# Optimization experiments

Measured on AMD Instinct MI355X. Metric: run time of the kernel, lower is better.

## Reference

```python
import jax, jax.numpy as jnp
import numpy as np

B, S, D = 1, 4096, 768
H = 12
HD = D // H  # 64


def setup_inputs() -> dict:
    key = jax.random.key(0)
    ks = jax.random.split(key, 6)
    sd = 1.0 / np.sqrt(D)
    return {
        "inputs": jax.random.normal(ks[0], (B, S, D), dtype=jnp.float32),
        "Wq": jax.random.uniform(ks[1], (D, D), jnp.float32, -sd, sd),
        "Wk": jax.random.uniform(ks[2], (D, D), jnp.float32, -sd, sd),
        "Wv": jax.random.uniform(ks[3], (D, D), jnp.float32, -sd, sd),
        "Wo": jax.random.uniform(ks[4], (D, D), jnp.float32, -sd, sd),
        "bo": jax.random.uniform(ks[5], (D,), jnp.float32, -sd, sd),
    }


def reference(inputs, Wq, Wk, Wv, Wo, bo):
    b, n, _ = inputs.shape
    # Linear layers (torch Linear: x @ W.T); W stored as [d_out, d_in]-equivalent here as [D, D] applied via x @ W.T
    q = inputs @ Wq.T  # [b, n, D]
    k = inputs @ Wk.T
    v = inputs @ Wv.T
    # [b, H, n, HD]
    q = q.reshape(b, n, H, HD).transpose(0, 2, 1, 3)
    k = k.reshape(b, n, H, HD).transpose(0, 2, 1, 3)
    v = v.reshape(b, n, H, HD).transpose(0, 2, 1, 3)
    scores = jnp.einsum("bhqd,bhkd->bhqk", q, k)
    causal = jnp.triu(jnp.ones((n, n), dtype=bool), k=1)
    scores = jnp.where(causal, -jnp.inf, scores)
    attn = jax.nn.softmax(scores / np.sqrt(HD), axis=-1)  # dropout p=0.0 -> identity
    ctx = jnp.einsum("bhqk,bhkd->bhqd", attn, v)
    ctx = ctx.transpose(0, 2, 1, 3).reshape(b, n, D)
    return ctx @ Wo.T + bo
```

## Files before the change

kernel.cpp:

```cpp
#include <hip/hip_runtime.h>
#include <math.h>

static constexpr int S_LEN  = 4096;
static constexpr int DMODEL = 768;
static constexpr int NHEAD  = 12;
static constexpr int HDIM   = 64;

typedef __attribute__((ext_vector_type(8))) short   bf16x8;
typedef __attribute__((ext_vector_type(4))) float   f32x4;
typedef __attribute__((ext_vector_type(8))) unsigned short us8;

__device__ __forceinline__ unsigned short f2b(float f) {
  union { float f; unsigned int u; } v; v.f = f;
  unsigned int u = v.u;
  return (unsigned short)((u + 0x7fffu + ((u >> 16) & 1u)) >> 16);
}

__device__ __forceinline__ float dpp_max16(float x) {
  float y;
  y = __int_as_float(__builtin_amdgcn_mov_dpp(__float_as_int(x), 0xB1, 0xf, 0xf, true)); x = fmaxf(x, y);
  y = __int_as_float(__builtin_amdgcn_mov_dpp(__float_as_int(x), 0x4E, 0xf, 0xf, true)); x = fmaxf(x, y);
  y = __int_as_float(__builtin_amdgcn_mov_dpp(__float_as_int(x), 0x124, 0xf, 0xf, true)); x = fmaxf(x, y);
  y = __int_as_float(__builtin_amdgcn_mov_dpp(__float_as_int(x), 0x128, 0xf, 0xf, true)); x = fmaxf(x, y);
  return x;
}
__device__ __forceinline__ float dpp_sum16(float x) {
  float y;
  y = __int_as_float(__builtin_amdgcn_mov_dpp(__float_as_int(x), 0xB1, 0xf, 0xf, true)); x += y;
  y = __int_as_float(__builtin_amdgcn_mov_dpp(__float_as_int(x), 0x4E, 0xf, 0xf, true)); x += y;
  y = __int_as_float(__builtin_amdgcn_mov_dpp(__float_as_int(x), 0x124, 0xf, 0xf, true)); x += y;
  y = __int_as_float(__builtin_amdgcn_mov_dpp(__float_as_int(x), 0x128, 0xf, 0xf, true)); x += y;
  return x;
}

__global__ __launch_bounds__(256)
void cvt_f2b_kern(const float* __restrict__ in, unsigned short* __restrict__ out, int n) {
  int i = (blockIdx.x * blockDim.x + threadIdx.x) * 8;
  if (i >= n) return;
  float4 a = *(const float4*)(in + i);
  float4 b = *(const float4*)(in + i + 4);
  ushort4 o0; o0.x = f2b(a.x); o0.y = f2b(a.y); o0.z = f2b(a.z); o0.w = f2b(a.w);
  ushort4 o1; o1.x = f2b(b.x); o1.y = f2b(b.y); o1.z = f2b(b.z); o1.w = f2b(b.w);
  *(ushort4*)(out + i)     = o0;
  *(ushort4*)(out + i + 4) = o1;
}

__global__ __launch_bounds__(256)
void cvt_f2b4_kern(const float* __restrict__ s0, const float* __restrict__ s1,
                   const float* __restrict__ s2, const float* __restrict__ s3,
                   unsigned short* __restrict__ d0, unsigned short* __restrict__ d1,
                   unsigned short* __restrict__ d2, unsigned short* __restrict__ d3,
                   int n) {
  const float* s; unsigned short* d;
  switch (blockIdx.y) {
    case 0: s = s0; d = d0; break;
    case 1: s = s1; d = d1; break;
    case 2: s = s2; d = d2; break;
    default: s = s3; d = d3; break;
  }
  int i = (blockIdx.x * blockDim.x + threadIdx.x) * 8;
  if (i >= n) return;
  float4 a = *(const float4*)(s + i);
  float4 b = *(const float4*)(s + i + 4);
  ushort4 o0; o0.x = f2b(a.x); o0.y = f2b(a.y); o0.z = f2b(a.z); o0.w = f2b(a.w);
  ushort4 o1; o1.x = f2b(b.x); o1.y = f2b(b.y); o1.z = f2b(b.z); o1.w = f2b(b.w);
  *(ushort4*)(d + i)     = o0;
  *(ushort4*)(d + i + 4) = o1;
}

__global__ __launch_bounds__(256)
void transpose_bf16(const unsigned short* __restrict__ in, unsigned short* __restrict__ out) {
  __shared__ __align__(16) unsigned short Ts[64][72];
  const int d0 = blockIdx.x * 64, s0 = blockIdx.y * 64;
  const int r = threadIdx.x >> 2, q = threadIdx.x & 3;
#pragma unroll
  for (int hh = 0; hh < 2; ++hh) {
    const int c8 = q + hh * 4;
    us8 v = *(const us8*)(in + (size_t)(s0 + r) * DMODEL + d0 + c8 * 8);
    *(us8*)(&Ts[r][c8 * 8]) = v;
  }
  __syncthreads();
#pragma unroll
  for (int hh = 0; hh < 2; ++hh) {
    const int sq = q + hh * 4;
    __align__(16) unsigned short tmp[8];
#pragma unroll
    for (int j = 0; j < 8; ++j) tmp[j] = Ts[sq * 8 + j][r];
    *(us8*)(out + (size_t)(d0 + r) * S_LEN + s0 + sq * 8) = *(us8*)tmp;
  }
}

template<int OUT_MODE>
__device__ __forceinline__
void gemm_body(const unsigned short* __restrict__ A, const unsigned short* __restrict__ B,
               const float* __restrict__ bias, void* __restrict__ Cout,
               int M, int N, int K, float scale, int bx, int by,
               unsigned short* As, unsigned short* Bs) {
  const int l  = threadIdx.x & 63;
  const int w  = threadIdx.x >> 6;
  const int wm = (w >> 1) * 32, wn = (w & 1) * 32;
  const int m0 = by * 64;
  const int n0 = bx * 64;
  const int lr = l & 15, lg = l >> 4;
  const int sr = threadIdx.x >> 2, sq = threadIdx.x & 3;

  f32x4 acc[2][2] = {};
  us8 areg[2], breg[2];

#pragma unroll
  for (int p = 0; p < 2; ++p) {
    const int c = sq + p * 4;
    areg[p] = *(const us8*)(A + (size_t)(m0 + sr) * K + c * 8);
    breg[p] = *(const us8*)(B + (size_t)(n0 + sr) * K + c * 8);
  }
#pragma unroll
  for (int p = 0; p < 2; ++p) {
    const int c = sq + p * 4;
    const int slot = ((c ^ (sr & 7)) * 8);
    *(us8*)(&As[sr * 64 + slot]) = areg[p];
    *(us8*)(&Bs[sr * 64 + slot]) = breg[p];
  }
  __syncthreads();

  const int nsteps = K / 64;
  for (int t = 0; t < nsteps; ++t) {
    const bool more = (t + 1 < nsteps);
    if (more) {
      const int kn = (t + 1) * 64;
#pragma unroll
      for (int p = 0; p < 2; ++p) {
        const int c = sq + p * 4;
        areg[p] = *(const us8*)(A + (size_t)(m0 + sr) * K + kn + c * 8);
        breg[p] = *(const us8*)(B + (size_t)(n0 + sr) * K + kn + c * 8);
      }
    }
#pragma unroll
    for (int kc = 0; kc < 2; ++kc) {
      const int cr = kc * 4 + lg;
      bf16x8 af[2], bfr[2];
#pragma unroll
      for (int mi = 0; mi < 2; ++mi) {
        const int row = wm + mi * 16 + lr;
        af[mi] = *(const bf16x8*)(&As[row * 64 + ((cr ^ (row & 7)) * 8)]);
      }
#pragma unroll
      for (int ni = 0; ni < 2; ++ni) {
        const int row = wn + ni * 16 + lr;
        bfr[ni] = *(const bf16x8*)(&Bs[row * 64 + ((cr ^ (row & 7)) * 8)]);
      }
#pragma unroll
      for (int mi = 0; mi < 2; ++mi)
#pragma unroll
        for (int ni = 0; ni < 2; ++ni)
          acc[mi][ni] = __builtin_amdgcn_mfma_f32_16x16x32_bf16(af[mi], bfr[ni], acc[mi][ni], 0, 0, 0);
    }
    __syncthreads();
    if (more) {
#pragma unroll
      for (int p = 0; p < 2; ++p) {
        const int c = sq + p * 4;
        const int slot = ((c ^ (sr & 7)) * 8);
        *(us8*)(&As[sr * 64 + slot]) = areg[p];
        *(us8*)(&Bs[sr * 64 + slot]) = breg[p];
      }
      __syncthreads();
    }
  }

  const int orow = (l >> 4) * 4;
#pragma unroll
  for (int mi = 0; mi < 2; ++mi)
#pragma unroll
    for (int ni = 0; ni < 2; ++ni) {
      const int col = n0 + wn + ni * 16 + lr;
      float bb = (OUT_MODE == 1) ? bias[col] : 0.f;
#pragma unroll
      for (int r = 0; r < 4; ++r) {
        const int row = m0 + wm + mi * 16 + orow + r;
        float v = acc[mi][ni][r] * scale;
        if (OUT_MODE == 0)
          ((unsigned short*)Cout)[(size_t)row * N + col] = f2b(v);
        else
          ((float*)Cout)[(size_t)row * N + col] = v + bb;
      }
    }
}

__global__ __launch_bounds__(256)
void gemm_qkv_lds(const unsigned short* __restrict__ X,
                  const unsigned short* __restrict__ Wq, const unsigned short* __restrict__ Wk,
                  const unsigned short* __restrict__ Wv,
                  unsigned short* __restrict__ Qh, unsigned short* __restrict__ Kh,
                  unsigned short* __restrict__ Vh) {
  __shared__ __align__(16) unsigned short As[64 * 64];
  __shared__ __align__(16) unsigned short Bs[64 * 64];
  const unsigned short* B; unsigned short* C; float scale;
  switch (blockIdx.z) {
    case 0:  B = Wq; C = Qh; scale = 0.125f; break;
    case 1:  B = Wk; C = Kh; scale = 1.0f;   break;
    default: B = Wv; C = Vh; scale = 1.0f;   break;
  }
  gemm_body<0>(X, B, nullptr, C, S_LEN, DMODEL, DMODEL, scale,
               blockIdx.x, blockIdx.y, As, Bs);
}

__global__ __launch_bounds__(256)
void gemm_lds_f32(const unsigned short* __restrict__ A, const unsigned short* __restrict__ B,
                  const float* __restrict__ bias, float* __restrict__ C) {
  __shared__ __align__(16) unsigned short As[64 * 64];
  __shared__ __align__(16) unsigned short Bs[64 * 64];
  gemm_body<1>(A, B, bias, C, S_LEN, DMODEL, DMODEL, 1.0f,
               blockIdx.x, blockIdx.y, As, Bs);
}

__global__ __launch_bounds__(256, 3)
void attn_fwd_mfma(const unsigned short* __restrict__ Q, const unsigned short* __restrict__ K,
                   const unsigned short* __restrict__ Vt, unsigned short* __restrict__ O) {
  __shared__ __align__(16) unsigned short Ks[2][64 * 64];
  __shared__ __align__(16) unsigned short Vs[2][64 * 64];
  __shared__ __align__(16) unsigned short Ps[4][2 * 16 * 64];

  const int item = blockIdx.x;
  int s;
  if (item < 256)      s = item;
  else if (item < 512) s = 767 - item;
  else                 s = item;
  const int qt = 63 - s / NHEAD;
  const int h  = s % NHEAD;
  const int q0 = qt * 64;
  const int tid = threadIdx.x;
  const int w = tid >> 6, l = tid & 63;
  const int lr = l & 15, lg = l >> 4;
  const int sr = tid >> 2, sq = tid & 3;

  bf16x8 qf[2];
#pragma unroll
  for (int kc = 0; kc < 2; ++kc)
    qf[kc] = *(const bf16x8*)(Q + (size_t)(q0 + w * 16 + lr) * DMODEL + h * HDIM + kc * 32 + lg * 8);

  f32x4 o_acc[4] = {};
  float m_i[4], l_i[4];
#pragma unroll
  for (int r = 0; r < 4; ++r) { m_i[r] = -1e30f; l_i[r] = 0.f; }

  const int nt2    = (qt + 2) >> 1;
  const int ntFull = (64 * qt >= 127) ? ((64 * qt - 127) / 128 + 1) : 0;

  us8 kreg[2][2], vreg[2][2];

#pragma unroll
  for (int hh = 0; hh < 2; ++hh)
#pragma unroll
    for (int p = 0; p < 2; ++p) {
      const int qw = sq + p * 4;
      kreg[hh][p] = *(const us8*)(K  + (size_t)(hh * 64 + sr) * DMODEL + h * HDIM + qw * 8);
      vreg[hh][p] = *(const us8*)(Vt + (size_t)(h * HDIM + sr) * S_LEN + hh * 64 + qw * 8);
    }
#pragma unroll
  for (int hh = 0; hh < 2; ++hh)
#pragma unroll
    for (int p = 0; p < 2; ++p) {
      const int qw = sq + p * 4;
      const int sw = (qw * 8) ^ ((sr & 7) * 8);
      *(us8*)(&Ks[hh][sr * 64 + sw]) = kreg[hh][p];
      *(us8*)(&Vs[hh][sr * 64 + sw]) = vreg[hh][p];
    }
  __syncthreads();

  for (int t = 0; t < nt2; ++t) {
    const int k0 = t * 128;
    const bool more = (t + 1 < nt2);
    const bool need_mask = (t >= ntFull);

    if (more) {
      const int k0n = k0 + 128;
#pragma unroll
      for (int hh = 0; hh < 2; ++hh)
#pragma unroll
        for (int p = 0; p < 2; ++p) {
          const int qw = sq + p * 4;
          kreg[hh][p] = *(const us8*)(K  + (size_t)(k0n + hh * 64 + sr) * DMODEL + h * HDIM + qw * 8);
          vreg[hh][p] = *(const us8*)(Vt + (size_t)(h * HDIM + sr) * S_LEN + k0n + hh * 64 + qw * 8);
        }
    }

    f32x4 sacc[2][4] = {};
#pragma unroll
    for (int hh = 0; hh < 2; ++hh)
#pragma unroll
      for (int kc = 0; kc < 2; ++kc)
#pragma unroll
        for (int cb = 0; cb < 4; ++cb) {
          const int kv = cb * 16 + lr;
          bf16x8 kf = *(const bf16x8*)(&Ks[hh][kv * 64 + ((kc * 32 + lg * 8) ^ ((kv & 7) * 8))]);
          sacc[hh][cb] = __builtin_amdgcn_mfma_f32_16x16x32_bf16(qf[kc], kf, sacc[hh][cb], 0, 0, 0);
        }

    float p[4][8];
#pragma unroll
    for (int r = 0; r < 4; ++r) {
      const int qg = q0 + w * 16 + lg * 4 + r;
      float sv[8];
#pragma unroll
      for (int hh = 0; hh < 2; ++hh)
#pragma unroll
        for (int cb = 0; cb < 4; ++cb)
          sv[hh * 4 + cb] = sacc[hh][cb][r];
      if (need_mask) {
#pragma unroll
        for (int hh = 0; hh < 2; ++hh)
#pragma unroll
          for (int cb = 0; cb < 4; ++cb) {
            const int kg = k0 + hh * 64 + cb * 16 + lr;
            if (kg > qg) sv[hh * 4 + cb] = -1e30f;
          }
      }
      float mt = fmaxf(fmaxf(fmaxf(sv[0], sv[1]), fmaxf(sv[2], sv[3])),
                       fmaxf(fmaxf(sv[4], sv[5]), fmaxf(sv[6], sv[7])));
      mt = dpp_max16(mt);
      const float mnew = fmaxf(m_i[r], mt);
      const float alpha = __expf(m_i[r] - mnew);
      m_i[r] = mnew;
      float rs = 0.f;
#pragma unroll
      for (int e = 0; e < 8; ++e) { p[r][e] = __expf(sv[e] - mnew); rs += p[r][e]; }
      rs = dpp_sum16(rs);
      l_i[r] = l_i[r] * alpha + rs;
#pragma unroll
      for (int db = 0; db < 4; ++db) o_acc[db][r] *= alpha;
    }

#pragma unroll
    for (int r = 0; r < 4; ++r) {
      const int qloc = lg * 4 + r;
#pragma unroll
      for (int hh = 0; hh < 2; ++hh)
#pragma unroll
        for (int cb = 0; cb < 4; ++cb) {
          const int kvl = cb * 16 + lr;
          Ps[w][hh * 1024 + qloc * 64 + (kvl ^ ((qloc & 7) * 8))] = f2b(p[r][hh * 4 + cb]);
        }
    }

#pragma unroll
    for (int hh = 0; hh < 2; ++hh)
#pragma unroll
      for (int kc = 0; kc < 2; ++kc) {
        bf16x8 pf = *(const bf16x8*)(&Ps[w][hh * 1024 + lr * 64 + ((kc * 32 + lg * 8) ^ ((lr & 7) * 8))]);
#pragma unroll
        for (int db = 0; db < 4; ++db) {
          const int d = db * 16 + lr;
          bf16x8 vf = *(const bf16x8*)(&Vs[hh][d * 64 + ((kc * 32 + lg * 8) ^ ((d & 7) * 8))]);
          o_acc[db] = __builtin_amdgcn_mfma_f32_16x16x32_bf16(pf, vf, o_acc[db], 0, 0, 0);
        }
      }

    __syncthreads();
    if (more) {
#pragma unroll
      for (int hh = 0; hh < 2; ++hh)
#pragma unroll
        for (int p = 0; p < 2; ++p) {
          const int qw = sq + p * 4;
          const int sw = (qw * 8) ^ ((sr & 7) * 8);
          *(us8*)(&Ks[hh][sr * 64 + sw]) = kreg[hh][p];
          *(us8*)(&Vs[hh][sr * 64 + sw]) = vreg[hh][p];
        }
      __syncthreads();
    }
  }

#pragma unroll
  for (int r = 0; r < 4; ++r) {
    const float inv = 1.f / l_i[r];
    const int row = q0 + w * 16 + lg * 4 + r;
#pragma unroll
    for (int db = 0; db < 4; ++db)
      O[(size_t)row * DMODEL + h * HDIM + db * 16 + lr] = f2b(o_acc[db][r] * inv);
  }
}

extern "C" void kernel_launch(void* const* d_in, const int* in_sizes, int n_in,
                              void* d_out, int out_size, void* d_ws, size_t ws_size,
                              hipStream_t stream) {
  const float* x  = (const float*)d_in[0];
  const float* Wq = (const float*)d_in[1];
  const float* Wk = (const float*)d_in[2];
  const float* Wv = (const float*)d_in[3];
  const float* Wo = (const float*)d_in[4];
  const float* bo = (const float*)d_in[5];
  float* out = (float*)d_out;

  const size_t SD = (size_t)S_LEN * DMODEL;
  const size_t DD = (size_t)DMODEL * DMODEL;

  unsigned short* xh   = (unsigned short*)d_ws;
  unsigned short* Wqh  = xh   + SD;
  unsigned short* Wkh  = Wqh  + DD;
  unsigned short* Wvh  = Wkh  + DD;
  unsigned short* Woh  = Wvh  + DD;
  unsigned short* Qh   = Woh  + DD;
  unsigned short* Kh   = Qh   + SD;
  unsigned short* Vh   = Kh   + SD;
  unsigned short* Vth  = Vh   + SD;
  unsigned short* ctxh = Vth  + SD;

  const dim3 blk(256);

  cvt_f2b_kern<<<dim3((int)(SD / 8 / 256)), blk, 0, stream>>>(x, xh, (int)SD);
  cvt_f2b4_kern<<<dim3((int)(DD / 8 / 256), 4), blk, 0, stream>>>(
      Wq, Wk, Wv, Wo, Wqh, Wkh, Wvh, Woh, (int)DD);

  gemm_qkv_lds<<<dim3(DMODEL / 64, S_LEN / 64, 3), blk, 0, stream>>>(
      xh, Wqh, Wkh, Wvh, Qh, Kh, Vh);

  transpose_bf16<<<dim3(DMODEL / 64, S_LEN / 64), blk, 0, stream>>>(Vh, Vth);

  attn_fwd_mfma<<<dim3(S_LEN / 64 * NHEAD), blk, 0, stream>>>(Qh, Kh, Vth, ctxh);

  gemm_lds_f32<<<dim3(DMODEL / 64, S_LEN / 64), blk, 0, stream>>>(ctxh, Woh, bo, out);
}
```

Before: 140.2 us.

## Use 128-row query tiles with 8 waves per attention block

Each attention block now covers 128 query rows with 512 threads (8 waves) instead of 64 rows with 256 threads, so every K/V tile loaded into LDS is reused by twice as many query rows and global K/V traffic is halved. The cooperative loads now use 8 lanes per row, and the block-to-tile mapping is changed to balance causal work across a grid half as large. Every tile now spans the full 128-key step, so only the diagonal tile needs masking, but fewer, larger blocks may reduce occupancy and load balance.

```diff
diff --git a/kernel.cpp b/kernel.cpp
--- a/kernel.cpp
+++ b/kernel.cpp
@@ -213,75 +213,66 @@
                blockIdx.x, blockIdx.y, As, Bs);
 }
 
-__global__ __launch_bounds__(256, 3)
+__global__ __launch_bounds__(512, 2)
 void attn_fwd_mfma(const unsigned short* __restrict__ Q, const unsigned short* __restrict__ K,
                    const unsigned short* __restrict__ Vt, unsigned short* __restrict__ O) {
   __shared__ __align__(16) unsigned short Ks[2][64 * 64];
   __shared__ __align__(16) unsigned short Vs[2][64 * 64];
-  __shared__ __align__(16) unsigned short Ps[4][2 * 16 * 64];
-
-  const int item = blockIdx.x;
-  int s;
-  if (item < 256)      s = item;
-  else if (item < 512) s = 767 - item;
-  else                 s = item;
-  const int qt = 63 - s / NHEAD;
-  const int h  = s % NHEAD;
-  const int q0 = qt * 64;
+  __shared__ __align__(16) unsigned short Ps[8][2 * 16 * 64];
+
+  const int pos = blockIdx.x;
+  int rank;
+  if (pos < 128)       rank = 128 + pos;
+  else if (pos < 256)  rank = pos - 128;
+  else                 rank = 383 - (pos - 256);
+  const int qtile = 31 - rank / NHEAD;
+  const int h     = rank % NHEAD;
+  const int q0b   = qtile * 128;
+
   const int tid = threadIdx.x;
   const int w = tid >> 6, l = tid & 63;
   const int lr = l & 15, lg = l >> 4;
-  const int sr = tid >> 2, sq = tid & 3;
+  const int sr = tid >> 3, sq = tid & 7;
 
   bf16x8 qf[2];
 #pragma unroll
   for (int kc = 0; kc < 2; ++kc)
-    qf[kc] = *(const bf16x8*)(Q + (size_t)(q0 + w * 16 + lr) * DMODEL + h * HDIM + kc * 32 + lg * 8);
+    qf[kc] = *(const bf16x8*)(Q + (size_t)(q0b + w * 16 + lr) * DMODEL + h * HDIM + kc * 32 + lg * 8);
 
   f32x4 o_acc[4] = {};
   float m_i[4], l_i[4];
 #pragma unroll
   for (int r = 0; r < 4; ++r) { m_i[r] = -1e30f; l_i[r] = 0.f; }
 
-  const int nt2    = (qt + 2) >> 1;
-  const int ntFull = (64 * qt >= 127) ? ((64 * qt - 127) / 128 + 1) : 0;
-
-  us8 kreg[2][2], vreg[2][2];
-
-#pragma unroll
-  for (int hh = 0; hh < 2; ++hh)
-#pragma unroll
-    for (int p = 0; p < 2; ++p) {
-      const int qw = sq + p * 4;
-      kreg[hh][p] = *(const us8*)(K  + (size_t)(hh * 64 + sr) * DMODEL + h * HDIM + qw * 8);
-      vreg[hh][p] = *(const us8*)(Vt + (size_t)(h * HDIM + sr) * S_LEN + hh * 64 + qw * 8);
-    }
-#pragma unroll
-  for (int hh = 0; hh < 2; ++hh)
-#pragma unroll
-    for (int p = 0; p < 2; ++p) {
-      const int qw = sq + p * 4;
-      const int sw = (qw * 8) ^ ((sr & 7) * 8);
-      *(us8*)(&Ks[hh][sr * 64 + sw]) = kreg[hh][p];
-      *(us8*)(&Vs[hh][sr * 64 + sw]) = vreg[hh][p];
-    }
+  const int nt = qtile + 1;
+
+  us8 kreg[2], vreg[2];
+
+#pragma unroll
+  for (int hh = 0; hh < 2; ++hh) {
+    kreg[hh] = *(const us8*)(K  + (size_t)(hh * 64 + sr) * DMODEL + h * HDIM + sq * 8);
+    vreg[hh] = *(const us8*)(Vt + (size_t)(h * HDIM + sr) * S_LEN + hh * 64 + sq * 8);
+  }
+#pragma unroll
+  for (int hh = 0; hh < 2; ++hh) {
+    const int sw = (sq * 8) ^ ((sr & 7) * 8);
+    *(us8*)(&Ks[hh][sr * 64 + sw]) = kreg[hh];
+    *(us8*)(&Vs[hh][sr * 64 + sw]) = vreg[hh];
+  }
   __syncthreads();
 
-  for (int t = 0; t < nt2; ++t) {
+  for (int t = 0; t < nt; ++t) {
     const int k0 = t * 128;
-    const bool more = (t + 1 < nt2);
-    const bool need_mask = (t >= ntFull);
+    const bool more = (t + 1 < nt);
+    const bool need_mask = (t == qtile);
 
     if (more) {
       const int k0n = k0 + 128;
 #pragma unroll
-      for (int hh = 0; hh < 2; ++hh)
-#pragma unroll
-        for (int p = 0; p < 2; ++p) {
-          const int qw = sq + p * 4;
-          kreg[hh][p] = *(const us8*)(K  + (size_t)(k0n + hh * 64 + sr) * DMODEL + h * HDIM + qw * 8);
-          vreg[hh][p] = *(const us8*)(Vt + (size_t)(h * HDIM + sr) * S_LEN + k0n + hh * 64 + qw * 8);
-        }
+      for (int hh = 0; hh < 2; ++hh) {
+        kreg[hh] = *(const us8*)(K  + (size_t)(k0n + hh * 64 + sr) * DMODEL + h * HDIM + sq * 8);
+        vreg[hh] = *(const us8*)(Vt + (size_t)(h * HDIM + sr) * S_LEN + k0n + hh * 64 + sq * 8);
+      }
     }
 
     f32x4 sacc[2][4] = {};
@@ -299,7 +290,7 @@
     float p[4][8];
 #pragma unroll
     for (int r = 0; r < 4; ++r) {
-      const int qg = q0 + w * 16 + lg * 4 + r;
+      const int qg = q0b + w * 16 + lg * 4 + r;
       float sv[8];
 #pragma unroll
       for (int hh = 0; hh < 2; ++hh)
@@ -358,14 +349,11 @@
     __syncthreads();
     if (more) {
 #pragma unroll
-      for (int hh = 0; hh < 2; ++hh)
-#pragma unroll
-        for (int p = 0; p < 2; ++p) {
-          const int qw = sq + p * 4;
-          const int sw = (qw * 8) ^ ((sr & 7) * 8);
-          *(us8*)(&Ks[hh][sr * 64 + sw]) = kreg[hh][p];
-          *(us8*)(&Vs[hh][sr * 64 + sw]) = vreg[hh][p];
-        }
+      for (int hh = 0; hh < 2; ++hh) {
+        const int sw = (sq * 8) ^ ((sr & 7) * 8);
+        *(us8*)(&Ks[hh][sr * 64 + sw]) = kreg[hh];
+        *(us8*)(&Vs[hh][sr * 64 + sw]) = vreg[hh];
+      }
       __syncthreads();
     }
   }
@@ -373,7 +361,7 @@
 #pragma unroll
   for (int r = 0; r < 4; ++r) {
     const float inv = 1.f / l_i[r];
-    const int row = q0 + w * 16 + lg * 4 + r;
+    const int row = q0b + w * 16 + lg * 4 + r;
 #pragma unroll
     for (int db = 0; db < 4; ++db)
       O[(size_t)row * DMODEL + h * HDIM + db * 16 + lr] = f2b(o_acc[db][r] * inv);
@@ -416,7 +404,7 @@
 
   transpose_bf16<<<dim3(DMODEL / 64, S_LEN / 64), blk, 0, stream>>>(Vh, Vth);
 
-  attn_fwd_mfma<<<dim3(S_LEN / 64 * NHEAD), blk, 0, stream>>>(Qh, Kh, Vth, ctxh);
+  attn_fwd_mfma<<<dim3(S_LEN / 128 * NHEAD), dim3(512), 0, stream>>>(Qh, Kh, Vth, ctxh);
 
   gemm_lds_f32<<<dim3(DMODEL / 64, S_LEN / 64), blk, 0, stream>>>(ctxh, Woh, bo, out);
 }
```

Result: slower. 151.0 us (+7.7%).

## Fold log2e into Q scale, use exp2, and skip rescale with lazy max

Applied to the files above, without the earlier changes.

The Q projection scale now includes log2(e), so the attention softmax can use the native exp2 instruction instead of __expf. The online-softmax rescale of the running output and sum is skipped wave-wide whenever every row's new tile max stays within 8 of the running max, which avoids per-tile alpha multiplies. Global-to-LDS loads are also remapped so each thread reads two adjacent 16-byte chunks instead of strided ones. The lazy-rescale threshold lets exponentials reach up to 2^8, a small risk to range and precision in exchange for less per-tile work.

```diff
diff --git a/kernel.cpp b/kernel.cpp
--- a/kernel.cpp
+++ b/kernel.cpp
@@ -109,13 +109,13 @@
 
 #pragma unroll
   for (int p = 0; p < 2; ++p) {
-    const int c = sq + p * 4;
+    const int c = sq * 2 + p;
     areg[p] = *(const us8*)(A + (size_t)(m0 + sr) * K + c * 8);
     breg[p] = *(const us8*)(B + (size_t)(n0 + sr) * K + c * 8);
   }
 #pragma unroll
   for (int p = 0; p < 2; ++p) {
-    const int c = sq + p * 4;
+    const int c = sq * 2 + p;
     const int slot = ((c ^ (sr & 7)) * 8);
     *(us8*)(&As[sr * 64 + slot]) = areg[p];
     *(us8*)(&Bs[sr * 64 + slot]) = breg[p];
@@ -129,7 +129,7 @@
       const int kn = (t + 1) * 64;
 #pragma unroll
       for (int p = 0; p < 2; ++p) {
-        const int c = sq + p * 4;
+        const int c = sq * 2 + p;
         areg[p] = *(const us8*)(A + (size_t)(m0 + sr) * K + kn + c * 8);
         breg[p] = *(const us8*)(B + (size_t)(n0 + sr) * K + kn + c * 8);
       }
@@ -158,7 +158,7 @@
     if (more) {
 #pragma unroll
       for (int p = 0; p < 2; ++p) {
-        const int c = sq + p * 4;
+        const int c = sq * 2 + p;
         const int slot = ((c ^ (sr & 7)) * 8);
         *(us8*)(&As[sr * 64 + slot]) = areg[p];
         *(us8*)(&Bs[sr * 64 + slot]) = breg[p];
@@ -196,7 +196,7 @@
   __shared__ __align__(16) unsigned short Bs[64 * 64];
   const unsigned short* B; unsigned short* C; float scale;
   switch (blockIdx.z) {
-    case 0:  B = Wq; C = Qh; scale = 0.125f; break;
+    case 0:  B = Wq; C = Qh; scale = 0.125f * 1.4426950408889634f; break;
     case 1:  B = Wk; C = Kh; scale = 1.0f;   break;
     default: B = Wv; C = Vh; scale = 1.0f;   break;
   }
@@ -252,7 +252,7 @@
   for (int hh = 0; hh < 2; ++hh)
 #pragma unroll
     for (int p = 0; p < 2; ++p) {
-      const int qw = sq + p * 4;
+      const int qw = sq * 2 + p;
       kreg[hh][p] = *(const us8*)(K  + (size_t)(hh * 64 + sr) * DMODEL + h * HDIM + qw * 8);
       vreg[hh][p] = *(const us8*)(Vt + (size_t)(h * HDIM + sr) * S_LEN + hh * 64 + qw * 8);
     }
@@ -260,7 +260,7 @@
   for (int hh = 0; hh < 2; ++hh)
 #pragma unroll
     for (int p = 0; p < 2; ++p) {
-      const int qw = sq + p * 4;
+      const int qw = sq * 2 + p;
       const int sw = (qw * 8) ^ ((sr & 7) * 8);
       *(us8*)(&Ks[hh][sr * 64 + sw]) = kreg[hh][p];
       *(us8*)(&Vs[hh][sr * 64 + sw]) = vreg[hh][p];
@@ -278,7 +278,7 @@
       for (int hh = 0; hh < 2; ++hh)
 #pragma unroll
         for (int p = 0; p < 2; ++p) {
-          const int qw = sq + p * 4;
+          const int qw = sq * 2 + p;
           kreg[hh][p] = *(const us8*)(K  + (size_t)(k0n + hh * 64 + sr) * DMODEL + h * HDIM + qw * 8);
           vreg[hh][p] = *(const us8*)(Vt + (size_t)(h * HDIM + sr) * S_LEN + k0n + hh * 64 + qw * 8);
         }
@@ -296,38 +296,51 @@
           sacc[hh][cb] = __builtin_amdgcn_mfma_f32_16x16x32_bf16(qf[kc], kf, sacc[hh][cb], 0, 0, 0);
         }
 
-    float p[4][8];
+    float sv[4][8], pm[4];
 #pragma unroll
     for (int r = 0; r < 4; ++r) {
       const int qg = q0 + w * 16 + lg * 4 + r;
-      float sv[8];
 #pragma unroll
       for (int hh = 0; hh < 2; ++hh)
 #pragma unroll
         for (int cb = 0; cb < 4; ++cb)
-          sv[hh * 4 + cb] = sacc[hh][cb][r];
+          sv[r][hh * 4 + cb] = sacc[hh][cb][r];
       if (need_mask) {
 #pragma unroll
         for (int hh = 0; hh < 2; ++hh)
 #pragma unroll
           for (int cb = 0; cb < 4; ++cb) {
             const int kg = k0 + hh * 64 + cb * 16 + lr;
-            if (kg > qg) sv[hh * 4 + cb] = -1e30f;
+            if (kg > qg) sv[r][hh * 4 + cb] = -1e30f;
           }
       }
-      float mt = fmaxf(fmaxf(fmaxf(sv[0], sv[1]), fmaxf(sv[2], sv[3])),
-                       fmaxf(fmaxf(sv[4], sv[5]), fmaxf(sv[6], sv[7])));
-      mt = dpp_max16(mt);
-      const float mnew = fmaxf(m_i[r], mt);
-      const float alpha = __expf(m_i[r] - mnew);
-      m_i[r] = mnew;
+      float mt = fmaxf(fmaxf(fmaxf(sv[r][0], sv[r][1]), fmaxf(sv[r][2], sv[r][3])),
+                       fmaxf(fmaxf(sv[r][4], sv[r][5]), fmaxf(sv[r][6], sv[r][7])));
+      pm[r] = dpp_max16(mt);
+    }
+
+    const int ok = (pm[0] <= m_i[0] + 8.f) && (pm[1] <= m_i[1] + 8.f) &&
+                   (pm[2] <= m_i[2] + 8.f) && (pm[3] <= m_i[3] + 8.f);
+    if (!__all(ok)) {
+#pragma unroll
+      for (int r = 0; r < 4; ++r) {
+        const float mnew = fmaxf(m_i[r], pm[r]);
+        const float alpha = __builtin_amdgcn_exp2f(m_i[r] - mnew);
+        m_i[r] = mnew;
+        l_i[r] *= alpha;
+#pragma unroll
+        for (int db = 0; db < 4; ++db) o_acc[db][r] *= alpha;
+      }
+    }
+
+    float p[4][8];
+#pragma unroll
+    for (int r = 0; r < 4; ++r) {
       float rs = 0.f;
 #pragma unroll
-      for (int e = 0; e < 8; ++e) { p[r][e] = __expf(sv[e] - mnew); rs += p[r][e]; }
+      for (int e = 0; e < 8; ++e) { p[r][e] = __builtin_amdgcn_exp2f(sv[r][e] - m_i[r]); rs += p[r][e]; }
       rs = dpp_sum16(rs);
-      l_i[r] = l_i[r] * alpha + rs;
-#pragma unroll
-      for (int db = 0; db < 4; ++db) o_acc[db][r] *= alpha;
+      l_i[r] += rs;
     }
 
 #pragma unroll
@@ -361,7 +374,7 @@
       for (int hh = 0; hh < 2; ++hh)
 #pragma unroll
         for (int p = 0; p < 2; ++p) {
-          const int qw = sq + p * 4;
+          const int qw = sq * 2 + p;
           const int sw = (qw * 8) ^ ((sr & 7) * 8);
           *(us8*)(&Ks[hh][sr * 64 + sw]) = kreg[hh][p];
           *(us8*)(&Vs[hh][sr * 64 + sw]) = vreg[hh][p];
```

Result: faster. 133.5 us (-4.7%).
